# Performance work log

Measured on AMD Instinct MI355X. Metric: run time of the kernel, lower is better.

The kernel has to match this reference:

```python
import jax, jax.numpy as jnp
import numpy as np

B, D_IN, D_EMB = 8192, 256, 128
N_EX, N_DUR = 16384, 64
N_TRAIN = 100000
THRESH = 1.0


def setup_inputs() -> dict:
    key = jax.random.key(0)
    ks = jax.random.split(key, 6)
    x = jax.random.normal(ks[0], (B, D_IN), jnp.float32)
    # small scales so pairwise distances straddle the threshold (realistic kernel regime)
    W = jax.random.normal(ks[1], (D_IN, D_EMB), jnp.float32) * 0.003
    b = jnp.zeros((D_EMB,), jnp.float32)
    E = jax.random.normal(ks[2], (N_EX, D_EMB), jnp.float32) * 0.05
    log_ev = jax.random.normal(ks[3], (N_EX, N_DUR), jnp.float32)
    log_cen = jax.random.normal(ks[4], (N_EX, N_DUR), jnp.float32)
    logit_h = jax.random.normal(ks[5], (N_DUR,), jnp.float32) - 3.0
    return {
        "input": x, "W": W, "b": b, "exemplar_embeddings": E,
        "log_exemplar_event_counts": log_ev,
        "log_exemplar_censor_counts": log_cen,
        "logit_baseline_hazard": logit_h,
    }


def _kernel_weights(x, W, b, E):
    # encoder (no_grad in original): single linear layer
    phi = x @ W + b  # [B, D_EMB]
    # cdist via Gram expansion; clamp tiny negatives from roundoff
    d2 = (jnp.sum(phi * phi, axis=1, keepdims=True)
          + jnp.sum(E * E, axis=1)[None, :]
          - 2.0 * (phi @ E.T))
    d2 = jnp.maximum(d2, 0.0)          # [B, N_EX] squared distances
    d = jnp.sqrt(d2)
    # threshold mask + exp kernel (matches exp(-distance**2))
    return jnp.where(d <= THRESH, jnp.exp(-d2), 0.0)


def reference(input, W, b, exemplar_embeddings,
              log_exemplar_event_counts, log_exemplar_censor_counts,
              logit_baseline_hazard):
    kw = jax.lax.stop_gradient(
        _kernel_weights(input, W, b, exemplar_embeddings))  # [B, N_EX]

    baseline_hazard = jax.nn.sigmoid(logit_baseline_hazard)  # [N_DUR]
    baseline_KM = jnp.exp(jnp.cumsum(jnp.log(1.0 - baseline_hazard + 1e-7)))

    ev = jnp.exp(log_exemplar_event_counts)    # [N_EX, N_DUR]
    cen = jnp.exp(log_exemplar_censor_counts)  # [N_EX, N_DUR]
    # reverse cumulative sum along durations = flip/cumsum/flip
    at_risk = jnp.flip(jnp.cumsum(jnp.flip(ev + cen, axis=1), axis=1), axis=1)
    pos = at_risk > 0
    hazards = jnp.where(pos, ev / jnp.where(pos, at_risk, 1.0), 0.0)
    exemplar_KM = jnp.exp(jnp.cumsum(jnp.log(1.0 - hazards + 1e-7), axis=1))

    gamma_n = jnp.exp(-(THRESH ** 2)) / N_TRAIN
    numer = kw @ exemplar_KM + gamma_n * baseline_KM[None, :]  # [B, N_DUR]
    denom = (jnp.sum(kw, axis=1) + gamma_n + 1e-12)[:, None]
    return jnp.clip(numer / denom, 1e-12, 1.0 - 1e-12)
```

## Files before the change

### kernel.cpp

```cpp
#include <hip/hip_runtime.h>

using short8  = __attribute__((ext_vector_type(8))) short;
using floatx4 = __attribute__((ext_vector_type(4))) float;

#define NB   8192
#define DIN  256
#define DE   128
#define NEX  16384
#define ND   64
#define ESPLIT 16
#define EPB  (NEX/ESPLIT)
#define TE   64
#define NTIL (EPB/TE)
#define GAMMA_N 3.6787944117144233e-06f

__device__ __forceinline__ unsigned short f2bf(float f) {
  unsigned int u = __float_as_uint(f);
  u += 0x7fffu + ((u >> 16) & 1u);
  return (unsigned short)(u >> 16);
}
__device__ __forceinline__ float bf2f(unsigned short h) {
  return __uint_as_float(((unsigned int)h) << 16);
}
__device__ __forceinline__ unsigned int pk_bf16(float a, float b) {
  unsigned int r;
  asm("v_cvt_pk_bf16_f32 %0, %1, %2" : "=v"(r) : "v"(a), "v"(b));
  return r;
}

__device__ __forceinline__ void gload_lds16(const void* g, void* l) {
  __builtin_amdgcn_global_load_lds(
      (const __attribute__((address_space(1))) void*)g,
      (__attribute__((address_space(3))) void*)l, 16, 0, 0);
}

__device__ __forceinline__ floatx4 mfma_bf16(short8 a, short8 b, floatx4 c) {
  return __builtin_amdgcn_mfma_f32_16x16x32_bf16(a, b, c, 0, 0, 0);
}

__global__ __launch_bounds__(256) void k_prep(
    const float* __restrict__ x, const float* __restrict__ W,
    const float* __restrict__ bias, unsigned short* __restrict__ phi_bf,
    float* __restrict__ pn,
    const float* __restrict__ E, unsigned short* __restrict__ E_bf,
    float* __restrict__ en,
    const float* __restrict__ lev, const float* __restrict__ lcen,
    const float* __restrict__ lh, unsigned short* __restrict__ KM_t,
    float* __restrict__ baseKM)
{
  __shared__ __align__(16) unsigned char smem[8192];
  const int bid = blockIdx.x;
  const int tid = threadIdx.x;

  if (bid < 1024) {
    const int rb = bid * 8;
    float* xs = (float*)smem;
    for (int i = tid; i < 8 * DIN / 4; i += 256)
      reinterpret_cast<float4*>(xs)[i] =
          reinterpret_cast<const float4*>(x + (size_t)rb * DIN)[i];
    __syncthreads();
    const int jt = tid & 31;
    const int rt = tid >> 5;
    float4 acc = *reinterpret_cast<const float4*>(&bias[jt * 4]);
    const float* xr = xs + rt * DIN;
    #pragma unroll 8
    for (int k = 0; k < DIN; ++k) {
      const float4 wv = *reinterpret_cast<const float4*>(&W[k * DE + jt * 4]);
      const float xv = xr[k];
      acc.x = fmaf(xv, wv.x, acc.x); acc.y = fmaf(xv, wv.y, acc.y);
      acc.z = fmaf(xv, wv.z, acc.z); acc.w = fmaf(xv, wv.w, acc.w);
    }
    const int row = rb + rt;
    const unsigned int p0 = pk_bf16(acc.x, acc.y);
    const unsigned int p1 = pk_bf16(acc.z, acc.w);
    *reinterpret_cast<uint2*>(phi_bf + (size_t)row * DE + jt * 4) =
        make_uint2(p0, p1);
    const float h0 = bf2f(p0 & 0xffff), h1 = bf2f(p0 >> 16);
    const float h2 = bf2f(p1 & 0xffff), h3 = bf2f(p1 >> 16);
    float s = h0 * h0 + h1 * h1 + h2 * h2 + h3 * h3;
    s += __shfl_xor(s, 1, 64);
    s += __shfl_xor(s, 2, 64);
    s += __shfl_xor(s, 4, 64);
    s += __shfl_xor(s, 8, 64);
    s += __shfl_xor(s, 16, 64);
    if (jt == 0) pn[row] = s;

  } else if (bid < 1536) {
    const int bb = bid - 1024;
    const int l  = tid & 63;
    const int row = bb * 32 + (tid >> 6) * 8 + (l >> 3);
    const int c0  = (l & 7) * 16;
    const float4* src = reinterpret_cast<const float4*>(E + (size_t)row * DE + c0);
    float4 v0 = src[0], v1 = src[1], v2 = src[2], v3 = src[3];
    unsigned int p[8];
    p[0] = pk_bf16(v0.x, v0.y); p[1] = pk_bf16(v0.z, v0.w);
    p[2] = pk_bf16(v1.x, v1.y); p[3] = pk_bf16(v1.z, v1.w);
    p[4] = pk_bf16(v2.x, v2.y); p[5] = pk_bf16(v2.z, v2.w);
    p[6] = pk_bf16(v3.x, v3.y); p[7] = pk_bf16(v3.z, v3.w);
    uint4* dst = reinterpret_cast<uint4*>(E_bf + (size_t)row * DE + c0);
    dst[0] = make_uint4(p[0], p[1], p[2], p[3]);
    dst[1] = make_uint4(p[4], p[5], p[6], p[7]);
    float s = 0.f;
    #pragma unroll
    for (int i = 0; i < 8; ++i) {
      const float lo = bf2f(p[i] & 0xffff), hi = bf2f(p[i] >> 16);
      s = fmaf(lo, lo, s); s = fmaf(hi, hi, s);
    }
    s += __shfl_xor(s, 1, 64);
    s += __shfl_xor(s, 2, 64);
    s += __shfl_xor(s, 4, 64);
    if ((l & 7) == 0) en[row] = s;

  } else {
    const int bb = bid - 1536;
    unsigned short (*sm)[65] = (unsigned short (*)[65])smem;
    const int t  = tid & 63;
    const int wv = tid >> 6;
    for (int ee = 0; ee < 8; ++ee) {
      const int el = wv * 8 + ee;
      const int e  = bb * 32 + el;
      const float ev = __expf(lev[e * ND + t]);
      const float cn = __expf(lcen[e * ND + t]);
      float s = ev + cn;
      #pragma unroll
      for (int off = 1; off < 64; off <<= 1) {
        const float o = __shfl(s, (t + off) & 63, 64);
        s += (t + off < 64) ? o : 0.0f;
      }
      const float haz = (s > 0.0f) ? (ev / s) : 0.0f;
      float lc = __logf(1.0f - haz + 1e-7f);
      #pragma unroll
      for (int off = 1; off < 64; off <<= 1) {
        const float o = __shfl(lc, (t - off) & 63, 64);
        lc += (t >= off) ? o : 0.0f;
      }
      sm[el][t] = f2bf(__expf(lc));
    }
    __syncthreads();
    const int t_out = tid >> 2, prt = tid & 3;
    unsigned short tmp[8];
    #pragma unroll
    for (int i = 0; i < 8; ++i) tmp[i] = sm[prt * 8 + i][t_out];
    *reinterpret_cast<short8*>(KM_t + (size_t)t_out * NEX + bb * 32 + prt * 8) =
        *reinterpret_cast<short8*>(&tmp[0]);
    if (bb == 0 && tid < 64) {
      const float h = 1.0f / (1.0f + __expf(-lh[t]));
      float l2 = __logf(1.0f - h + 1e-7f);
      #pragma unroll
      for (int off = 1; off < 64; off <<= 1) {
        const float o = __shfl(l2, (t - off) & 63, 64);
        l2 += (t >= off) ? o : 0.0f;
      }
      baseKM[t] = __expf(l2);
    }
  }
}

__global__ __launch_bounds__(256, 4) void k_fused(
    const unsigned short* __restrict__ phi_bf, const float* __restrict__ pn,
    const unsigned short* __restrict__ E_bf, const float* __restrict__ en,
    const unsigned short* __restrict__ KM_t,
    float* __restrict__ numer_p, float* __restrict__ denom_p)
{
  __shared__ __align__(16) unsigned char E_lds[16384];
  __shared__ __align__(16) unsigned char KM_lds[8192];
  __shared__ __align__(16) unsigned char kw_lds[8192];

  const int tid = threadIdx.x;
  const int w   = tid >> 6;
  const int l   = tid & 63;
  const int lr  = l & 15;
  const int g   = l >> 4;
  const int rowbase = blockIdx.y * 128 + w * 32;
  const int ebase0  = blockIdx.x * EPB;
  const int swz  = (lr & 7) << 4;
  const int swz2 = ((lr >> 1) & 3) << 4;

  short8 phiB[2][4];
  float  pnf[2];
  #pragma unroll
  for (int n = 0; n < 2; ++n) {
    const int r = rowbase + n * 16 + lr;
    #pragma unroll
    for (int kq = 0; kq < 4; ++kq)
      phiB[n][kq] = *reinterpret_cast<const short8*>(phi_bf + r * DE + kq * 32 + g * 8);
    pnf[n] = pn[r];
  }

  floatx4 c2[4][2];
  #pragma unroll
  for (int m2 = 0; m2 < 4; ++m2)
    #pragma unroll
    for (int n = 0; n < 2; ++n) c2[m2][n] = (floatx4){0.f, 0.f, 0.f, 0.f};
  float dn[2] = {0.f, 0.f};

  for (int it = 0; it < NTIL; ++it) {
    const int ebase = ebase0 + it * TE;
    __syncthreads();
    #pragma unroll
    for (int i = 0; i < 4; ++i) {
      const int c    = w * 4 + i;
      const int row  = c * 4 + (l >> 4);
      const int colB = (l & 15) * 16;
      gload_lds16((const char*)E_bf + (size_t)(ebase + row) * 256 +
                      (colB ^ ((row & 7) << 4)),
                  &E_lds[c * 1024]);
    }
    #pragma unroll
    for (int i = 0; i < 2; ++i) {
      const int c    = w * 2 + i;
      const int trow = c * 8 + (l >> 3);
      const int colB = (l & 7) * 16;
      gload_lds16((const char*)KM_t + (size_t)trow * (NEX * 2) + ebase * 2 +
                      (colB ^ ((trow & 7) << 4)),
                  &KM_lds[c * 1024]);
    }
    __syncthreads();

    #pragma unroll
    for (int h = 0; h < 2; ++h) {
      #pragma unroll
      for (int mm = 0; mm < 2; ++mm) {
        const int m = 2 * h + mm;
        short8 ea[4];
        #pragma unroll
        for (int kq = 0; kq < 4; ++kq)
          ea[kq] = *reinterpret_cast<const short8*>(
              &E_lds[(m * 16 + lr) * 256 + ((kq * 64 + g * 16) ^ swz)]);
        floatx4 c1[2];
        c1[0] = (floatx4){0.f, 0.f, 0.f, 0.f};
        c1[1] = (floatx4){0.f, 0.f, 0.f, 0.f};
        #pragma unroll
        for (int kq = 0; kq < 4; ++kq) {
          c1[0] = mfma_bf16(ea[kq], phiB[0][kq], c1[0]);
          c1[1] = mfma_bf16(ea[kq], phiB[1][kq], c1[1]);
        }
        const floatx4 en4 = *reinterpret_cast<const floatx4*>(&en[ebase + m * 16 + g * 4]);
        #pragma unroll
        for (int n = 0; n < 2; ++n) {
          float kwv[4];
          #pragma unroll
          for (int rg = 0; rg < 4; ++rg) {
            const float d2 = en4[rg] + pnf[n] - 2.0f * c1[n][rg];
            kwv[rg] = (d2 <= 1.0f) ? __expf(-d2) : 0.0f;
            dn[n] += kwv[rg];
          }
          const unsigned int pk0 = pk_bf16(kwv[0], kwv[1]);
          const unsigned int pk1 = pk_bf16(kwv[2], kwv[3]);
          const unsigned long long pk = (unsigned long long)pk0 |
                                        ((unsigned long long)pk1 << 32);
          *reinterpret_cast<unsigned long long*>(
              &kw_lds[w * 2048 + (n * 16 + lr) * 64 + ((mm * 32 + g * 8) ^ swz2)]) = pk;
        }
      }
      short8 kwB[2];
      #pragma unroll
      for (int n = 0; n < 2; ++n)
        kwB[n] = *reinterpret_cast<const short8*>(
            &kw_lds[w * 2048 + (n * 16 + lr) * 64 + ((g * 16) ^ swz2)]);
      #pragma unroll
      for (int m2 = 0; m2 < 4; ++m2) {
        const short8 kma = *reinterpret_cast<const short8*>(
            &KM_lds[(m2 * 16 + lr) * 128 + ((h * 64 + g * 16) ^ swz)]);
        c2[m2][0] = mfma_bf16(kma, kwB[0], c2[m2][0]);
        c2[m2][1] = mfma_bf16(kma, kwB[1], c2[m2][1]);
      }
    }
  }

  #pragma unroll
  for (int n = 0; n < 2; ++n) {
    float v = dn[n];
    v += __shfl_xor(v, 16, 64);
    v += __shfl_xor(v, 32, 64);
    if (l < 16) denom_p[(size_t)blockIdx.x * NB + rowbase + n * 16 + lr] = v;
  }
  float* np = numer_p + ((size_t)blockIdx.x * NB + rowbase) * ND;
  #pragma unroll
  for (int n = 0; n < 2; ++n)
    #pragma unroll
    for (int m2 = 0; m2 < 4; ++m2)
      *reinterpret_cast<floatx4*>(&np[(n * 16 + lr) * ND + m2 * 16 + g * 4]) =
          c2[m2][n];
}

__global__ __launch_bounds__(256) void k_finalize(
    const float* __restrict__ numer_p, const float* __restrict__ denom_p,
    const float* __restrict__ baseKM, float* __restrict__ out)
{
  const int idx = blockIdx.x * 256 + threadIdx.x;
  const int b = idx >> 6;
  const int t = idx & 63;
  float num = 0.f, den = 0.f;
  #pragma unroll
  for (int s = 0; s < ESPLIT; ++s) {
    num += numer_p[(size_t)s * NB * ND + idx];
    den += denom_p[(size_t)s * NB + b];
  }
  num += GAMMA_N * baseKM[t];
  den += GAMMA_N + 1e-12f;
  float r = num / den;
  r = fminf(fmaxf(r, 1e-12f), 1.0f - 1e-12f);
  out[idx] = r;
}

extern "C" void kernel_launch(void* const* d_in, const int* in_sizes, int n_in,
                              void* d_out, int out_size, void* d_ws, size_t ws_size,
                              hipStream_t stream)
{
  const float* x    = (const float*)d_in[0];
  const float* W    = (const float*)d_in[1];
  const float* bias = (const float*)d_in[2];
  const float* E    = (const float*)d_in[3];
  const float* lev  = (const float*)d_in[4];
  const float* lcen = (const float*)d_in[5];
  const float* lh   = (const float*)d_in[6];
  float* out = (float*)d_out;

  char* ws = (char*)d_ws;
  size_t off = 0;
  auto alloc = [&](size_t bytes) -> void* {
    void* p = ws + off;
    off += (bytes + 255) & ~(size_t)255;
    return p;
  };
  unsigned short* phi_bf  = (unsigned short*)alloc((size_t)NB * DE * 2);
  unsigned short* E_bf    = (unsigned short*)alloc((size_t)NEX * DE * 2);
  unsigned short* KM_t    = (unsigned short*)alloc((size_t)ND * NEX * 2);
  float* pn       = (float*)alloc((size_t)NB * 4);
  float* en       = (float*)alloc((size_t)NEX * 4);
  float* baseKM   = (float*)alloc((size_t)ND * 4);
  float* numer_p  = (float*)alloc((size_t)ESPLIT * NB * ND * 4);
  float* denom_p  = (float*)alloc((size_t)ESPLIT * NB * 4);

  k_prep<<<2048, 256, 0, stream>>>(x, W, bias, phi_bf, pn,
                                   E, E_bf, en,
                                   lev, lcen, lh, KM_t, baseKM);
  k_fused<<<dim3(ESPLIT, NB / 128), 256, 0, stream>>>(phi_bf, pn, E_bf, en, KM_t,
                                                      numer_p, denom_p);
  k_finalize<<<(NB * ND) / 256, 256, 0, stream>>>(numer_p, denom_p, baseKM, out);
}
```

Before: 189.8 us.

## Double exemplar split, store bf16 partial numerators, restructure encoder GEMM tiling

Raises the exemplar split from 16 to 32 so the fused kernel launches twice as many blocks. Partial numerators are stored as packed bf16 in an MFMA-native order, and the finalize kernel remaps indices to read them, roughly halving partial-sum traffic per split. The encoder in k_prep now computes 32 rows per block with 16 register accumulators per thread, reusing each W load across rows, and uses fewer blocks. The trade-off is reduced precision in the partial sums and a finalize kernel that reads twice as many splits.

```diff
diff --git a/kernel.cpp b/kernel.cpp
--- a/kernel.cpp
+++ b/kernel.cpp
@@ -8,7 +8,7 @@
 #define DE   128
 #define NEX  16384
 #define ND   64
-#define ESPLIT 16
+#define ESPLIT 32
 #define EPB  (NEX/ESPLIT)
 #define TE   64
 #define NTIL (EPB/TE)
@@ -48,45 +48,48 @@
     const float* __restrict__ lh, unsigned short* __restrict__ KM_t,
     float* __restrict__ baseKM)
 {
-  __shared__ __align__(16) unsigned char smem[8192];
+  __shared__ float xs[32 * DIN];
+  __shared__ float part[32][2];
+  __shared__ unsigned short sm[32][65];
   const int bid = blockIdx.x;
   const int tid = threadIdx.x;
 
-  if (bid < 1024) {
-    const int rb = bid * 8;
-    float* xs = (float*)smem;
-    for (int i = tid; i < 8 * DIN / 4; i += 256)
+  if (bid < 256) {
+    const int rb = bid * 32;
+    for (int i = tid; i < 32 * DIN / 4; i += 256)
       reinterpret_cast<float4*>(xs)[i] =
           reinterpret_cast<const float4*>(x + (size_t)rb * DIN)[i];
     __syncthreads();
-    const int jt = tid & 31;
-    const int rt = tid >> 5;
-    float4 acc = *reinterpret_cast<const float4*>(&bias[jt * 4]);
-    const float* xr = xs + rt * DIN;
-    #pragma unroll 8
+    const int j  = tid & 127;
+    const int rh = tid >> 7;
+    const float bj = bias[j];
+    float acc[16];
+    #pragma unroll
+    for (int r = 0; r < 16; ++r) acc[r] = bj;
     for (int k = 0; k < DIN; ++k) {
-      const float4 wv = *reinterpret_cast<const float4*>(&W[k * DE + jt * 4]);
-      const float xv = xr[k];
-      acc.x = fmaf(xv, wv.x, acc.x); acc.y = fmaf(xv, wv.y, acc.y);
-      acc.z = fmaf(xv, wv.z, acc.z); acc.w = fmaf(xv, wv.w, acc.w);
-    }
-    const int row = rb + rt;
-    const unsigned int p0 = pk_bf16(acc.x, acc.y);
-    const unsigned int p1 = pk_bf16(acc.z, acc.w);
-    *reinterpret_cast<uint2*>(phi_bf + (size_t)row * DE + jt * 4) =
-        make_uint2(p0, p1);
-    const float h0 = bf2f(p0 & 0xffff), h1 = bf2f(p0 >> 16);
-    const float h2 = bf2f(p1 & 0xffff), h3 = bf2f(p1 >> 16);
-    float s = h0 * h0 + h1 * h1 + h2 * h2 + h3 * h3;
-    s += __shfl_xor(s, 1, 64);
-    s += __shfl_xor(s, 2, 64);
-    s += __shfl_xor(s, 4, 64);
-    s += __shfl_xor(s, 8, 64);
-    s += __shfl_xor(s, 16, 64);
-    if (jt == 0) pn[row] = s;
-
-  } else if (bid < 1536) {
-    const int bb = bid - 1024;
+      const float wv = W[k * DE + j];
+      #pragma unroll
+      for (int r = 0; r < 16; ++r)
+        acc[r] = fmaf(xs[(rh * 16 + r) * DIN + k], wv, acc[r]);
+    }
+    const int lane = tid & 63;
+    const int jh   = (tid >> 6) & 1;
+    #pragma unroll
+    for (int r = 0; r < 16; ++r) {
+      const int row = rh * 16 + r;
+      const unsigned short hb = f2bf(acc[r]);
+      phi_bf[(size_t)(rb + row) * DE + j] = hb;
+      const float hf = bf2f(hb);
+      float sq = hf * hf;
+      #pragma unroll
+      for (int off = 1; off < 64; off <<= 1) sq += __shfl_xor(sq, off, 64);
+      if (lane == 0) part[row][jh] = sq;
+    }
+    __syncthreads();
+    if (tid < 32) pn[rb + tid] = part[tid][0] + part[tid][1];
+
+  } else if (bid < 768) {
+    const int bb = bid - 256;
     const int l  = tid & 63;
     const int row = bb * 32 + (tid >> 6) * 8 + (l >> 3);
     const int c0  = (l & 7) * 16;
@@ -112,8 +115,7 @@
     if ((l & 7) == 0) en[row] = s;
 
   } else {
-    const int bb = bid - 1536;
-    unsigned short (*sm)[65] = (unsigned short (*)[65])smem;
+    const int bb = bid - 768;
     const int t  = tid & 63;
     const int wv = tid >> 6;
     for (int ee = 0; ee < 8; ++ee) {
@@ -160,7 +162,7 @@
     const unsigned short* __restrict__ phi_bf, const float* __restrict__ pn,
     const unsigned short* __restrict__ E_bf, const float* __restrict__ en,
     const unsigned short* __restrict__ KM_t,
-    float* __restrict__ numer_p, float* __restrict__ denom_p)
+    uint4* __restrict__ numer_p, float* __restrict__ denom_p)
 {
   __shared__ __align__(16) unsigned char E_lds[16384];
   __shared__ __align__(16) unsigned char KM_lds[8192];
@@ -275,26 +277,32 @@
     v += __shfl_xor(v, 32, 64);
     if (l < 16) denom_p[(size_t)blockIdx.x * NB + rowbase + n * 16 + lr] = v;
   }
-  float* np = numer_p + ((size_t)blockIdx.x * NB + rowbase) * ND;
-  #pragma unroll
-  for (int n = 0; n < 2; ++n)
-    #pragma unroll
-    for (int m2 = 0; m2 < 4; ++m2)
-      *reinterpret_cast<floatx4*>(&np[(n * 16 + lr) * ND + m2 * 16 + g * 4]) =
-          c2[m2][n];
+  #pragma unroll
+  for (int n = 0; n < 2; ++n) {
+    const size_t rbase = ((size_t)blockIdx.x * NB + rowbase + n * 16 + lr) * 8;
+    #pragma unroll
+    for (int p = 0; p < 2; ++p)
+      numer_p[rbase + p * 4 + g] =
+          make_uint4(pk_bf16(c2[2 * p][n][0],     c2[2 * p][n][1]),
+                     pk_bf16(c2[2 * p][n][2],     c2[2 * p][n][3]),
+                     pk_bf16(c2[2 * p + 1][n][0], c2[2 * p + 1][n][1]),
+                     pk_bf16(c2[2 * p + 1][n][2], c2[2 * p + 1][n][3]));
+  }
 }
 
 __global__ __launch_bounds__(256) void k_finalize(
-    const float* __restrict__ numer_p, const float* __restrict__ denom_p,
+    const unsigned short* __restrict__ numer_p, const float* __restrict__ denom_p,
     const float* __restrict__ baseKM, float* __restrict__ out)
 {
   const int idx = blockIdx.x * 256 + threadIdx.x;
   const int b = idx >> 6;
   const int t = idx & 63;
+  const int m2 = t >> 4, g = (t >> 2) & 3, rg = t & 3;
+  const int pos = (m2 >> 1) * 32 + g * 8 + (m2 & 1) * 4 + rg;
   float num = 0.f, den = 0.f;
   #pragma unroll
   for (int s = 0; s < ESPLIT; ++s) {
-    num += numer_p[(size_t)s * NB * ND + idx];
+    num += bf2f(numer_p[(size_t)s * NB * ND + (size_t)b * ND + pos]);
     den += denom_p[(size_t)s * NB + b];
   }
   num += GAMMA_N * baseKM[t];
@@ -330,13 +338,14 @@
   float* pn       = (float*)alloc((size_t)NB * 4);
   float* en       = (float*)alloc((size_t)NEX * 4);
   float* baseKM   = (float*)alloc((size_t)ND * 4);
-  float* numer_p  = (float*)alloc((size_t)ESPLIT * NB * ND * 4);
+  uint4* numer_p  = (uint4*)alloc((size_t)ESPLIT * NB * ND * 2);
   float* denom_p  = (float*)alloc((size_t)ESPLIT * NB * 4);
 
-  k_prep<<<2048, 256, 0, stream>>>(x, W, bias, phi_bf, pn,
+  k_prep<<<1280, 256, 0, stream>>>(x, W, bias, phi_bf, pn,
                                    E, E_bf, en,
                                    lev, lcen, lh, KM_t, baseKM);
   k_fused<<<dim3(ESPLIT, NB / 128), 256, 0, stream>>>(phi_bf, pn, E_bf, en, KM_t,
                                                       numer_p, denom_p);
-  k_finalize<<<(NB * ND) / 256, 256, 0, stream>>>(numer_p, denom_p, baseKM, out);
-}
+  k_finalize<<<(NB * ND) / 256, 256, 0, stream>>>((const unsigned short*)numer_p,
+                                                  denom_p, baseKM, out);
+}
```

Result: faster. 184.4 us (-2.9%).
